# Performance work log

Measured on AMD Instinct MI355X. Metric: run time of the kernel, lower is better.

Reference implementation:

```python
import jax, jax.numpy as jnp
import numpy as np

V, E, H, B, S = 50000, 256, 256, 64, 2048


def setup_inputs() -> dict:
    key = jax.random.key(0)
    ks = jax.random.split(key, 13)
    u = lambda k, shape: jax.random.uniform(k, shape, jnp.float32) - 0.5
    return {
        "inp": jax.random.randint(ks[0], (B,), 0, V, dtype=jnp.int64),
        "hidden": jax.random.normal(ks[1], (1, B, H), jnp.float32),
        "encoder_outputs": jax.random.normal(ks[2], (B, S, H), jnp.float32),
        "emb": jax.random.normal(ks[3], (V, E), jnp.float32),          # nn.Embedding weight
        "U": u(ks[4], (H, H)),
        "W": u(ks[5], (H, H)),
        "v": u(ks[6], (H, 1)),
        "W_ih": u(ks[7], (H, E)),   # RNN weight_ih_l0
        "W_hh": u(ks[8], (H, H)),   # RNN weight_hh_l0
        "b_ih": u(ks[9], (H,)),
        "b_hh": u(ks[10], (H,)),
        "W_out": u(ks[11], (V, H)),  # output Linear weight
        "b_out": u(ks[12], (V,)),
    }


def reference(inp, hidden, encoder_outputs, emb, U, W, v,
              W_ih, W_hh, b_ih, b_hh, W_out, b_out):
    # embedding lookup: (B, E)
    x = emb[inp]
    word_embs = x[:, None, :]                         # (B, 1, E)
    # Bahdanau additive attention (get_context)
    summed = jnp.tanh(word_embs @ U + encoder_outputs @ W)   # (B, S, H)
    e_ij = summed @ v                                        # (B, S, 1)
    alpha = jax.nn.softmax(e_ij, axis=1)                     # (B, S, 1)
    context = jnp.sum(alpha * encoder_outputs, axis=1)       # (B, H)
    # single tanh-RNN step; NOTE: original code feeds context as initial hidden,
    # ignoring the `hidden` argument when attention is enabled.
    h_new = jnp.tanh(x @ W_ih.T + b_ih + context @ W_hh.T + b_hh)  # (B, H)
    logits = h_new @ W_out.T + b_out                               # (B, V)
    return logits, h_new[None]                                     # hidden: (1, B, H)
```

## Files before the change

### kernel.cpp

```cpp
#include <hip/hip_runtime.h>
#include <hip/hip_bf16.h>
#include <math.h>

#define V_ 50000
#define E_ 256
#define H_ 256
#define B_ 64
#define S_ 2048
#define NCHK 32

typedef __attribute__((ext_vector_type(4))) float f32x4;
typedef __attribute__((ext_vector_type(16))) float f32x16;
typedef __attribute__((ext_vector_type(8))) __bf16 bf16x8;

static __device__ __forceinline__ f32x4 mfma16(bf16x8 a, bf16x8 b, f32x4 c) {
  return __builtin_amdgcn_mfma_f32_16x16x32_bf16(a, b, c, 0, 0, 0);
}
static __device__ __forceinline__ f32x16 mfma32(bf16x8 a, bf16x8 b, f32x16 c) {
  return __builtin_amdgcn_mfma_f32_32x32x16_bf16(a, b, c, 0, 0, 0);
}
static __device__ __forceinline__ float fast_tanh(float x) {
  const float e2 = __expf(2.0f * x);
  return 1.0f - 2.0f / (e2 + 1.0f);
}

__global__ __launch_bounds__(256) void prep_k(
    const int* __restrict__ inp, const float* __restrict__ emb,
    const float* __restrict__ U, const float* __restrict__ W_ih,
    const float* __restrict__ b_ih, const float* __restrict__ b_hh,
    float* __restrict__ xU, float* __restrict__ xWih) {
  const int b = blockIdx.x, h = threadIdx.x;
  __shared__ float xs[H_];
  xs[h] = emb[(size_t)inp[b] * E_ + h];
  __syncthreads();
  float au = 0.f, aw = 0.f;
  const float* __restrict__ wir = W_ih + (size_t)h * E_;
  for (int k = 0; k < H_; k += 4) {
    const float4 x4 = *reinterpret_cast<const float4*>(&xs[k]);
    const float4 w4 = *reinterpret_cast<const float4*>(wir + k);
    aw = fmaf(x4.x, w4.x, aw); aw = fmaf(x4.y, w4.y, aw);
    aw = fmaf(x4.z, w4.z, aw); aw = fmaf(x4.w, w4.w, aw);
    au = fmaf(x4.x, U[(size_t)(k + 0) * H_ + h], au);
    au = fmaf(x4.y, U[(size_t)(k + 1) * H_ + h], au);
    au = fmaf(x4.z, U[(size_t)(k + 2) * H_ + h], au);
    au = fmaf(x4.w, U[(size_t)(k + 3) * H_ + h], au);
  }
  xU[b * H_ + h] = au;
  xWih[b * H_ + h] = aw + b_ih[h] + b_hh[h];
}

__global__ __launch_bounds__(256) void prep_w(
    const float* __restrict__ W, __bf16* __restrict__ wt2) {
  const int idx = blockIdx.x * 256 + threadIdx.x;
  const int k = idx >> 8, col = idx & 255;
  wt2[((size_t)(k >> 3) * 256 + col) * 8 + (k & 7)] = (__bf16)W[(size_t)k * H_ + col];
}

__global__ __launch_bounds__(512, 2) void attn_fused(
    const float* __restrict__ enc, const __bf16* __restrict__ wt2,
    const float* __restrict__ xU, const float* __restrict__ vv,
    float* __restrict__ ctxp, float* __restrict__ mlout) {
  const int t = threadIdx.x;
  const int w = t >> 6, l = t & 63, l31 = l & 31, h5 = l >> 5;

  __shared__ __bf16 Wl[32 * 256 * 8];
  __shared__ float ered[256];
  __shared__ float wgt[4][64];
  __shared__ float mlL[4][2];

  {
    const bf16x8* __restrict__ src = reinterpret_cast<const bf16x8*>(wt2);
    bf16x8* dst = reinterpret_cast<bf16x8*>(Wl);
#pragma unroll
    for (int i = 0; i < 16; ++i) dst[i * 512 + t] = src[i * 512 + t];
  }
  float xu[8], vw[8];
  __syncthreads();

#pragma unroll 1
  for (int uu = 0; uu < 2; ++uu) {
    const int unit = blockIdx.x * 2 + uu;
    const int b = unit >> 3;
    const int sidx = unit & 7;
    const int s0 = sidx * 256;

    const float* __restrict__ encA =
        enc + ((size_t)b * S_ + s0 + w * 32 + l31) * H_ + h5 * 8;

    f32x16 acc[8];
#pragma unroll
    for (int cf = 0; cf < 8; ++cf) acc[cf] = (f32x16)(0.f);

    float4 af[2][2];
    af[0][0] = *reinterpret_cast<const float4*>(encA);
    af[0][1] = *reinterpret_cast<const float4*>(encA + 4);

#pragma unroll
    for (int ks = 0; ks < 16; ++ks) {
      const int cb = ks & 1;
      if (ks < 15) {
        af[cb ^ 1][0] = *reinterpret_cast<const float4*>(encA + (ks + 1) * 16);
        af[cb ^ 1][1] = *reinterpret_cast<const float4*>(encA + (ks + 1) * 16 + 4);
      }
      bf16x8 bb[8];
      const int koct = ks * 2 + h5;
#pragma unroll
      for (int cf = 0; cf < 8; ++cf)
        bb[cf] = *reinterpret_cast<const bf16x8*>(
            &Wl[((size_t)koct * 256 + cf * 32 + l31) * 8]);
      bf16x8 ahi, alo;
      {
        const float xa[8] = {af[cb][0].x, af[cb][0].y, af[cb][0].z, af[cb][0].w,
                             af[cb][1].x, af[cb][1].y, af[cb][1].z, af[cb][1].w};
#pragma unroll
        for (int j = 0; j < 8; ++j) {
          const __bf16 hh = (__bf16)xa[j];
          ahi[j] = hh;
          alo[j] = (__bf16)(xa[j] - (float)hh);
        }
      }
#pragma unroll
      for (int cf = 0; cf < 8; ++cf) acc[cf] = mfma32(ahi, bb[cf], acc[cf]);
#pragma unroll
      for (int cf = 0; cf < 8; ++cf) acc[cf] = mfma32(alo, bb[cf], acc[cf]);
    }

#pragma unroll
    for (int cf = 0; cf < 8; ++cf) {
      const int col = cf * 32 + l31;
      xu[cf] = xU[b * H_ + col];
      vw[cf] = vv[col];
    }
    float rs[16];
#pragma unroll
    for (int reg = 0; reg < 16; ++reg) {
      float s = 0.f;
#pragma unroll
      for (int cf = 0; cf < 8; ++cf)
        s += fast_tanh(xu[cf] + acc[cf][reg]) * vw[cf];
      rs[reg] = s;
    }
#pragma unroll
    for (int o = 1; o < 32; o <<= 1)
#pragma unroll
      for (int reg = 0; reg < 16; ++reg)
        rs[reg] += __shfl_xor(rs[reg], o);
    if (l31 == 0) {
#pragma unroll
      for (int reg = 0; reg < 16; ++reg)
        ered[w * 32 + (reg & 3) + 8 * (reg >> 2) + 4 * h5] = rs[reg];
    }
    __syncthreads();

    if (t < 256) {
      const int cidx = t >> 6, rr = t & 63;
      const float es = ered[cidx * 64 + rr];
      float m = es;
#pragma unroll
      for (int o = 1; o < 64; o <<= 1) m = fmaxf(m, __shfl_xor(m, o));
      const float we = __expf(es - m);
      float ls = we;
#pragma unroll
      for (int o = 1; o < 64; o <<= 1) ls += __shfl_xor(ls, o);
      wgt[cidx][rr] = we;
      if (rr == 0) { mlL[cidx][0] = m; mlL[cidx][1] = ls; }
    }
    __syncthreads();

#pragma unroll
    for (int it = 0; it < 2; ++it) {
      const int cc = (t >> 8) + it * 2;
      const int h = t & 255;
      const float* __restrict__ ep = enc + ((size_t)b * S_ + s0 + cc * 64) * H_ + h;
      float a = 0.f;
#pragma unroll 8
      for (int s = 0; s < 64; ++s) a = fmaf(wgt[cc][s], ep[(size_t)s * H_], a);
      ctxp[((size_t)(sidx * 4 + cc) * B_ + b) * H_ + h] = a;
    }
    if (t < 8) {
      const int cc = t >> 1;
      mlout[((sidx * 4 + cc) * B_ + b) * 2 + (t & 1)] = mlL[cc][t & 1];
    }
    __syncthreads();
  }
}

__global__ __launch_bounds__(256) void combine_hnew(
    const float* __restrict__ ctxp, const float* __restrict__ mlout,
    const float* __restrict__ xWih, const float* __restrict__ W_hh,
    float* __restrict__ out_h, __bf16* __restrict__ hn) {
  const int b = blockIdx.x, h = threadIdx.x;
  __shared__ float cs[H_];
  float M = -3.4e38f;
#pragma unroll
  for (int cc = 0; cc < NCHK; ++cc) M = fmaxf(M, mlout[(cc * B_ + b) * 2]);
  float num = 0.f, den = 0.f;
#pragma unroll
  for (int cc = 0; cc < NCHK; ++cc) {
    const float mw = __expf(mlout[(cc * B_ + b) * 2] - M);
    den = fmaf(mw, mlout[(cc * B_ + b) * 2 + 1], den);
    num = fmaf(mw, ctxp[((size_t)cc * B_ + b) * H_ + h], num);
  }
  cs[h] = num / den;
  __syncthreads();
  const float* __restrict__ wr = W_hh + (size_t)h * H_;
  float a = xWih[b * H_ + h];
  for (int k = 0; k < H_; k += 4) {
    const float4 w4 = *reinterpret_cast<const float4*>(wr + k);
    const float4 c4 = *reinterpret_cast<const float4*>(&cs[k]);
    a = fmaf(c4.x, w4.x, a); a = fmaf(c4.y, w4.y, a);
    a = fmaf(c4.z, w4.z, a); a = fmaf(c4.w, w4.w, a);
  }
  const float hv = fast_tanh(a);
  out_h[b * H_ + h] = hv;
  hn[b * H_ + h] = (__bf16)hv;
}

__global__ __launch_bounds__(256) void logits_mfma(
    const float* __restrict__ Wout, const float* __restrict__ bout,
    const __bf16* __restrict__ hn, float* __restrict__ logits) {
  const int v0 = blockIdx.x * 64;
  const int t = threadIdx.x;
  const int wv = t >> 6, l = t & 63, l15 = l & 15, lg = l >> 4;

  __shared__ __bf16 Wsub[8][64][32];

  {
    const int srow = t >> 2, sg = t & 3;
    const int wslot = (sg + (srow >> 1)) & 3;
    const int vc = (v0 + srow) < V_ ? (v0 + srow) : (V_ - 1);
    const float* __restrict__ wr = Wout + (size_t)vc * H_ + sg * 8;
#pragma unroll
    for (int ks = 0; ks < 8; ++ks) {
      const float4 f0 = *reinterpret_cast<const float4*>(wr + ks * 32);
      const float4 f1 = *reinterpret_cast<const float4*>(wr + ks * 32 + 4);
      const float xv[8] = {f0.x, f0.y, f0.z, f0.w, f1.x, f1.y, f1.z, f1.w};
      bf16x8 h8;
#pragma unroll
      for (int j = 0; j < 8; ++j) h8[j] = (__bf16)xv[j];
      *reinterpret_cast<bf16x8*>(&Wsub[ks][srow][wslot * 8]) = h8;
    }
  }
  __syncthreads();

  f32x4 acc[4];
#pragma unroll
  for (int i = 0; i < 4; ++i) acc[i] = (f32x4)(0.f);
  const int colb = wv * 16 + l15;
#pragma unroll
  for (int k = 0; k < 8; ++k) {
    const bf16x8 bfrag = *reinterpret_cast<const bf16x8*>(hn + (size_t)colb * H_ + k * 32 + lg * 8);
    bf16x8 ah[4];
#pragma unroll
    for (int rf = 0; rf < 4; ++rf) {
      const int rr = rf * 16 + l15;
      const int slot = (lg + (rr >> 1)) & 3;
      ah[rf] = *reinterpret_cast<const bf16x8*>(&Wsub[k][rr][slot * 8]);
    }
#pragma unroll
    for (int rf = 0; rf < 4; ++rf)
      acc[rf] = mfma16(ah[rf], bfrag, acc[rf]);
  }
#pragma unroll
  for (int rf = 0; rf < 4; ++rf) {
    const int v = v0 + rf * 16 + lg * 4;
    if (v < V_) {
      const float4 bo = *reinterpret_cast<const float4*>(bout + v);
      float4 o;
      o.x = acc[rf][0] + bo.x; o.y = acc[rf][1] + bo.y;
      o.z = acc[rf][2] + bo.z; o.w = acc[rf][3] + bo.w;
      *reinterpret_cast<float4*>(logits + (size_t)colb * V_ + v) = o;
    }
  }
}

extern "C" void kernel_launch(void* const* d_in, const int* in_sizes, int n_in,
                              void* d_out, int out_size, void* d_ws, size_t ws_size,
                              hipStream_t stream) {
  const int*   inp  = (const int*)  d_in[0];
  const float* enc  = (const float*)d_in[2];
  const float* emb  = (const float*)d_in[3];
  const float* U    = (const float*)d_in[4];
  const float* W    = (const float*)d_in[5];
  const float* v    = (const float*)d_in[6];
  const float* W_ih = (const float*)d_in[7];
  const float* W_hh = (const float*)d_in[8];
  const float* b_ih = (const float*)d_in[9];
  const float* b_hh = (const float*)d_in[10];
  const float* Wout = (const float*)d_in[11];
  const float* bout = (const float*)d_in[12];

  float* logits = (float*)d_out;
  float* out_h  = logits + (size_t)B_ * V_;

  float* ws    = (float*)d_ws;
  __bf16* wt2  = (__bf16*)ws;
  float* xU    = ws + 32768;
  float* xWih  = xU + B_ * H_;
  float* ctxp  = xWih + B_ * H_;
  float* mlout = ctxp + (size_t)NCHK * B_ * H_;
  __bf16* hn   = (__bf16*)(mlout + NCHK * B_ * 2);

  prep_k<<<dim3(B_), dim3(256), 0, stream>>>(inp, emb, U, W_ih, b_ih, b_hh, xU, xWih);
  prep_w<<<dim3(H_ * H_ / 256), dim3(256), 0, stream>>>(W, wt2);
  attn_fused<<<dim3(256), dim3(512), 0, stream>>>(enc, wt2, xU, v, ctxp, mlout);
  combine_hnew<<<dim3(B_), dim3(256), 0, stream>>>(ctxp, mlout, xWih, W_hh, out_h, hn);
  logits_mfma<<<dim3((V_ + 63) / 64), dim3(256), 0, stream>>>(Wout, bout, hn, logits);
}
```

Before: 110.9 us.

## Split attention into 1024 smaller blocks with column-split warps and no LDS weight staging

Each attention block now handles 128 sequence rows of one batch, not two 256-row units. The grid grows from 256 to 1024 blocks and launch bounds move to 4 blocks per SM. Warps split into 4 row groups by 2 column halves, so each warp holds 4 accumulators instead of 8. The 128KB LDS copy of the bf16 W is removed and B fragments are read straight from global/L2. Per-half tanh partial sums are combined in shared memory, and A loads are prefetched two steps ahead. The aim is higher occupancy and less register and LDS pressure, at the cost of more repeated W reads through cache. NCHK stays 32 (16 blocks × 2 chunks), so combine is unchanged.

```diff
diff --git a/kernel.cpp b/kernel.cpp
--- a/kernel.cpp
+++ b/kernel.cpp
@@ -56,132 +56,119 @@
   wt2[((size_t)(k >> 3) * 256 + col) * 8 + (k & 7)] = (__bf16)W[(size_t)k * H_ + col];
 }
 
-__global__ __launch_bounds__(512, 2) void attn_fused(
+__global__ __launch_bounds__(512, 4) void attn_fused(
     const float* __restrict__ enc, const __bf16* __restrict__ wt2,
     const float* __restrict__ xU, const float* __restrict__ vv,
     float* __restrict__ ctxp, float* __restrict__ mlout) {
   const int t = threadIdx.x;
   const int w = t >> 6, l = t & 63, l31 = l & 31, h5 = l >> 5;
-
-  __shared__ __bf16 Wl[32 * 256 * 8];
-  __shared__ float ered[256];
-  __shared__ float wgt[4][64];
-  __shared__ float mlL[4][2];
+  const int rg = w >> 1, cg = w & 1;
+
+  __shared__ float ered[2][128];
+  __shared__ float wgt[2][64];
+  __shared__ float mlL[2][2];
+
+  const int ridx = blockIdx.x;
+  const int b = blockIdx.y;
+  const int s0 = ridx * 128;
+
+  const float* __restrict__ encA =
+      enc + ((size_t)b * S_ + s0 + rg * 32 + l31) * H_ + h5 * 8;
+
+  f32x16 acc[4];
+#pragma unroll
+  for (int cf = 0; cf < 4; ++cf) acc[cf] = (f32x16)(0.f);
+
+  float4 af[2][2];
+  af[0][0] = *reinterpret_cast<const float4*>(encA);
+  af[0][1] = *reinterpret_cast<const float4*>(encA + 4);
+  af[1][0] = *reinterpret_cast<const float4*>(encA + 16);
+  af[1][1] = *reinterpret_cast<const float4*>(encA + 20);
+
+#pragma unroll
+  for (int ks = 0; ks < 16; ++ks) {
+    const int ca = ks & 1;
+    bf16x8 ahi, alo;
+    {
+      const float4 c0 = af[ca][0], c1 = af[ca][1];
+      const float xa[8] = {c0.x, c0.y, c0.z, c0.w, c1.x, c1.y, c1.z, c1.w};
+#pragma unroll
+      for (int j = 0; j < 8; ++j) {
+        const __bf16 hh = (__bf16)xa[j];
+        ahi[j] = hh;
+        alo[j] = (__bf16)(xa[j] - (float)hh);
+      }
+    }
+    if (ks < 14) {
+      af[ca][0] = *reinterpret_cast<const float4*>(encA + (ks + 2) * 16);
+      af[ca][1] = *reinterpret_cast<const float4*>(encA + (ks + 2) * 16 + 4);
+    }
+    bf16x8 bb[4];
+    const int koct = ks * 2 + h5;
+#pragma unroll
+    for (int cf = 0; cf < 4; ++cf)
+      bb[cf] = *reinterpret_cast<const bf16x8*>(
+          wt2 + ((size_t)koct * 256 + cg * 128 + cf * 32 + l31) * 8);
+#pragma unroll
+    for (int cf = 0; cf < 4; ++cf) acc[cf] = mfma32(ahi, bb[cf], acc[cf]);
+#pragma unroll
+    for (int cf = 0; cf < 4; ++cf) acc[cf] = mfma32(alo, bb[cf], acc[cf]);
+  }
+
+  float xu[4], vw[4];
+#pragma unroll
+  for (int cf = 0; cf < 4; ++cf) {
+    const int col = cg * 128 + cf * 32 + l31;
+    xu[cf] = xU[b * H_ + col];
+    vw[cf] = vv[col];
+  }
+  float rs[16];
+#pragma unroll
+  for (int reg = 0; reg < 16; ++reg) {
+    float s = 0.f;
+#pragma unroll
+    for (int cf = 0; cf < 4; ++cf)
+      s += fast_tanh(xu[cf] + acc[cf][reg]) * vw[cf];
+    rs[reg] = s;
+  }
+#pragma unroll
+  for (int o = 1; o < 32; o <<= 1)
+#pragma unroll
+    for (int reg = 0; reg < 16; ++reg)
+      rs[reg] += __shfl_xor(rs[reg], o);
+  if (l31 == 0) {
+#pragma unroll
+    for (int reg = 0; reg < 16; ++reg)
+      ered[cg][rg * 32 + (reg & 3) + 8 * (reg >> 2) + 4 * h5] = rs[reg];
+  }
+  __syncthreads();
+
+  if (t < 128) {
+    const int cc = t >> 6, rr = t & 63;
+    const float es = ered[0][cc * 64 + rr] + ered[1][cc * 64 + rr];
+    float m = es;
+#pragma unroll
+    for (int o = 1; o < 64; o <<= 1) m = fmaxf(m, __shfl_xor(m, o));
+    const float we = __expf(es - m);
+    float ls = we;
+#pragma unroll
+    for (int o = 1; o < 64; o <<= 1) ls += __shfl_xor(ls, o);
+    wgt[cc][rr] = we;
+    if (rr == 0) { mlL[cc][0] = m; mlL[cc][1] = ls; }
+  }
+  __syncthreads();
 
   {
-    const bf16x8* __restrict__ src = reinterpret_cast<const bf16x8*>(wt2);
-    bf16x8* dst = reinterpret_cast<bf16x8*>(Wl);
-#pragma unroll
-    for (int i = 0; i < 16; ++i) dst[i * 512 + t] = src[i * 512 + t];
-  }
-  float xu[8], vw[8];
-  __syncthreads();
-
-#pragma unroll 1
-  for (int uu = 0; uu < 2; ++uu) {
-    const int unit = blockIdx.x * 2 + uu;
-    const int b = unit >> 3;
-    const int sidx = unit & 7;
-    const int s0 = sidx * 256;
-
-    const float* __restrict__ encA =
-        enc + ((size_t)b * S_ + s0 + w * 32 + l31) * H_ + h5 * 8;
-
-    f32x16 acc[8];
-#pragma unroll
-    for (int cf = 0; cf < 8; ++cf) acc[cf] = (f32x16)(0.f);
-
-    float4 af[2][2];
-    af[0][0] = *reinterpret_cast<const float4*>(encA);
-    af[0][1] = *reinterpret_cast<const float4*>(encA + 4);
-
-#pragma unroll
-    for (int ks = 0; ks < 16; ++ks) {
-      const int cb = ks & 1;
-      if (ks < 15) {
-        af[cb ^ 1][0] = *reinterpret_cast<const float4*>(encA + (ks + 1) * 16);
-        af[cb ^ 1][1] = *reinterpret_cast<const float4*>(encA + (ks + 1) * 16 + 4);
-      }
-      bf16x8 bb[8];
-      const int koct = ks * 2 + h5;
-#pragma unroll
-      for (int cf = 0; cf < 8; ++cf)
-        bb[cf] = *reinterpret_cast<const bf16x8*>(
-            &Wl[((size_t)koct * 256 + cf * 32 + l31) * 8]);
-      bf16x8 ahi, alo;
-      {
-        const float xa[8] = {af[cb][0].x, af[cb][0].y, af[cb][0].z, af[cb][0].w,
-                             af[cb][1].x, af[cb][1].y, af[cb][1].z, af[cb][1].w};
-#pragma unroll
-        for (int j = 0; j < 8; ++j) {
-          const __bf16 hh = (__bf16)xa[j];
-          ahi[j] = hh;
-          alo[j] = (__bf16)(xa[j] - (float)hh);
-        }
-      }
-#pragma unroll
-      for (int cf = 0; cf < 8; ++cf) acc[cf] = mfma32(ahi, bb[cf], acc[cf]);
-#pragma unroll
-      for (int cf = 0; cf < 8; ++cf) acc[cf] = mfma32(alo, bb[cf], acc[cf]);
-    }
-
-#pragma unroll
-    for (int cf = 0; cf < 8; ++cf) {
-      const int col = cf * 32 + l31;
-      xu[cf] = xU[b * H_ + col];
-      vw[cf] = vv[col];
-    }
-    float rs[16];
-#pragma unroll
-    for (int reg = 0; reg < 16; ++reg) {
-      float s = 0.f;
-#pragma unroll
-      for (int cf = 0; cf < 8; ++cf)
-        s += fast_tanh(xu[cf] + acc[cf][reg]) * vw[cf];
-      rs[reg] = s;
-    }
-#pragma unroll
-    for (int o = 1; o < 32; o <<= 1)
-#pragma unroll
-      for (int reg = 0; reg < 16; ++reg)
-        rs[reg] += __shfl_xor(rs[reg], o);
-    if (l31 == 0) {
-#pragma unroll
-      for (int reg = 0; reg < 16; ++reg)
-        ered[w * 32 + (reg & 3) + 8 * (reg >> 2) + 4 * h5] = rs[reg];
-    }
-    __syncthreads();
-
-    if (t < 256) {
-      const int cidx = t >> 6, rr = t & 63;
-      const float es = ered[cidx * 64 + rr];
-      float m = es;
-#pragma unroll
-      for (int o = 1; o < 64; o <<= 1) m = fmaxf(m, __shfl_xor(m, o));
-      const float we = __expf(es - m);
-      float ls = we;
-#pragma unroll
-      for (int o = 1; o < 64; o <<= 1) ls += __shfl_xor(ls, o);
-      wgt[cidx][rr] = we;
-      if (rr == 0) { mlL[cidx][0] = m; mlL[cidx][1] = ls; }
-    }
-    __syncthreads();
-
-#pragma unroll
-    for (int it = 0; it < 2; ++it) {
-      const int cc = (t >> 8) + it * 2;
-      const int h = t & 255;
-      const float* __restrict__ ep = enc + ((size_t)b * S_ + s0 + cc * 64) * H_ + h;
-      float a = 0.f;
+    const int cc = t >> 8, h = t & 255;
+    const float* __restrict__ ep = enc + ((size_t)b * S_ + s0 + cc * 64) * H_ + h;
+    float a = 0.f;
 #pragma unroll 8
-      for (int s = 0; s < 64; ++s) a = fmaf(wgt[cc][s], ep[(size_t)s * H_], a);
-      ctxp[((size_t)(sidx * 4 + cc) * B_ + b) * H_ + h] = a;
-    }
-    if (t < 8) {
-      const int cc = t >> 1;
-      mlout[((sidx * 4 + cc) * B_ + b) * 2 + (t & 1)] = mlL[cc][t & 1];
-    }
-    __syncthreads();
+    for (int s = 0; s < 64; ++s) a = fmaf(wgt[cc][s], ep[(size_t)s * H_], a);
+    ctxp[((size_t)(ridx * 2 + cc) * B_ + b) * H_ + h] = a;
+  }
+  if (t < 4) {
+    const int cc = t >> 1;
+    mlout[((ridx * 2 + cc) * B_ + b) * 2 + (t & 1)] = mlL[cc][t & 1];
   }
 }
 
@@ -303,7 +290,7 @@
 
   prep_k<<<dim3(B_), dim3(256), 0, stream>>>(inp, emb, U, W_ih, b_ih, b_hh, xU, xWih);
   prep_w<<<dim3(H_ * H_ / 256), dim3(256), 0, stream>>>(W, wt2);
-  attn_fused<<<dim3(256), dim3(512), 0, stream>>>(enc, wt2, xU, v, ctxp, mlout);
+  attn_fused<<<dim3(16, B_), dim3(512), 0, stream>>>(enc, wt2, xU, v, ctxp, mlout);
   combine_hnew<<<dim3(B_), dim3(256), 0, stream>>>(ctxp, mlout, xWih, W_hh, out_h, hn);
   logits_mfma<<<dim3((V_ + 63) / 64), dim3(256), 0, stream>>>(Wout, bout, hn, logits);
 }
```

New measurement: 116.2 us. 4.8% more time.
